# Optimization experiments

Measured on AMD Instinct MI355X. Metric: run time of the kernel, lower is better.

The kernel has to match this reference:

```python
import jax, jax.numpy as jnp
import numpy as np

N, G, S = 51200, 128, 400  # nodes, graphs, nodes-per-graph
E, IN, H, OUT = 819200, 128, 128, 10


def _graph_conv(x, src, dst, W_rel, b_rel, W_root):
    # PyG GraphConv (aggr='add'): lin_rel(sum_{j->i} x_j) + lin_root(x_i)
    agg = jax.ops.segment_sum(x[src], dst, num_segments=N)  # [N, d]
    return agg @ W_rel + b_rel + x @ W_root


def _mixup(x, lam, perm):
    return x * lam + (1.0 - lam) * x[perm]


def setup_inputs() -> dict:
    key = jax.random.key(0)
    ks = jax.random.split(key, 12)
    rng = np.random.default_rng(0)

    x0 = jax.random.normal(ks[0], (N, IN), dtype=jnp.float32)
    edge_index = jax.random.randint(ks[1], (2, E), 0, N, dtype=jnp.int64)
    lam = jax.random.uniform(ks[2], (1,), dtype=jnp.float32)
    ptr = jnp.arange(0, N + 1, S, dtype=jnp.int64)            # [G+1]
    batch = jnp.repeat(jnp.arange(G, dtype=jnp.int64), S)     # [N]

    def seg_perm():
        return jnp.asarray(np.concatenate(
            [g * S + rng.permutation(S) for g in range(G)]), dtype=jnp.int64)

    perm1, perm2, perm3 = seg_perm(), seg_perm(), seg_perm()

    def lin(k, fan_in, fan_out):
        bound = 1.0 / np.sqrt(fan_in)
        return jax.random.uniform(k, (fan_in, fan_out), jnp.float32, -bound, bound)

    params = {
        'W1_rel': lin(ks[3], IN, H), 'b1_rel': jnp.zeros((H,), jnp.float32),
        'W1_root': lin(ks[4], IN, H),
        'W2_rel': lin(ks[5], H, H), 'b2_rel': jnp.zeros((H,), jnp.float32),
        'W2_root': lin(ks[6], H, H),
        'W_lin': lin(ks[7], H, OUT), 'b_lin': jnp.zeros((OUT,), jnp.float32),
    }
    return dict(x0=x0, edge_index=edge_index, lam=lam, ptr=ptr, batch=batch,
                perm1=perm1, perm2=perm2, perm3=perm3, **params)


def reference(x0, edge_index, lam, ptr, batch, perm1, perm2, perm3,
              W1_rel, b1_rel, W1_root, W2_rel, b2_rel, W2_root, W_lin, b_lin):
    src, dst = edge_index[0], edge_index[1]
    l = lam[0]

    x1 = jax.nn.relu(_graph_conv(x0, src, dst, W1_rel, b1_rel, W1_root))
    x1 = _mixup(x1, l, perm1)  # dropout p=0.4 is identity in eval mode

    x2 = jax.nn.relu(_graph_conv(x1, src, dst, W2_rel, b2_rel, W2_root))
    x2 = _mixup(x2, l, perm2)

    # NOTE: original forward reuses conv2 for the third layer (conv3 unused)
    x3 = jax.nn.relu(_graph_conv(x2, src, dst, W2_rel, b2_rel, W2_root))
    x3 = _mixup(x3, l, perm3)

    pooled = jax.ops.segment_sum(x3, batch, num_segments=G)  # [G, H]
    logits = pooled @ W_lin + b_lin                          # [G, OUT]
    return jax.nn.log_softmax(logits, axis=-1)
```

## Files before the change

### kernel.cpp

```cpp
#include <hip/hip_runtime.h>

#define N_NODES 51200
#define N_EDGES 819200
#define HDIM 128
#define AK 256
#define NGRAPH 128
#define SEG 400
#define NOUT 10
#define SLOT 64

typedef unsigned short ushort_t;
typedef unsigned int uint_t;
typedef __attribute__((ext_vector_type(8))) short bf16x8;
typedef __attribute__((ext_vector_type(16))) float f32x16;

static __device__ __forceinline__ unsigned short f2bf(float f) {
    unsigned int u = __float_as_uint(f);
    unsigned int r = (u + 0x7fffu + ((u >> 16) & 1u)) >> 16;
    return (unsigned short)r;
}
static __device__ __forceinline__ float bf2f(unsigned short h) {
    return __uint_as_float(((unsigned int)h) << 16);
}


__global__ void k_scatter(const int* __restrict__ src, const int* __restrict__ dst,
                          int* __restrict__ cnt, ushort_t* __restrict__ col2) {
    int base = blockIdx.x * 1024 + threadIdx.x;
    int d[4], p[4];
#pragma unroll
    for (int k = 0; k < 4; ++k) d[k] = dst[base + k * 256];
#pragma unroll
    for (int k = 0; k < 4; ++k) p[k] = atomicAdd(&cnt[d[k]], 1);
#pragma unroll
    for (int k = 0; k < 4; ++k)
        col2[(size_t)d[k] * SLOT + p[k]] = (ushort_t)src[base + k * 256];
}


__global__ void k_prep(const float* __restrict__ x, ushort_t* __restrict__ Abuf,
                       const float* __restrict__ W1rel, const float* __restrict__ W1root,
                       const float* __restrict__ W2rel, const float* __restrict__ W2root,
                       ushort_t* __restrict__ Wfrag1, ushort_t* __restrict__ Wfrag2,
                       float* __restrict__ pooled) {
    int b = blockIdx.x;
    if (b < 6400) {
        int idx = b * 256 + threadIdx.x;
        int row = idx >> 5;
        int c4 = (idx & 31) * 4;
        float4 v = *(const float4*)(x + (size_t)row * HDIM + c4);
        ushort4 h;
        h.x = f2bf(v.x); h.y = f2bf(v.y); h.z = f2bf(v.z); h.w = f2bf(v.w);
        *(ushort4*)(Abuf + (size_t)row * AK + HDIM + c4) = h;
    } else if (b < 6656) {
        int w2 = (b >= 6528);
        int tid = (b - (w2 ? 6528 : 6400)) * 256 + threadIdx.x;
        const float* Wrel  = w2 ? W2rel : W1rel;
        const float* Wroot = w2 ? W2root : W1root;
        ushort_t* dstF     = w2 ? Wfrag2 : Wfrag1;
        int j = tid & 7;
        int l = (tid >> 3) & 63;
        int s = (tid >> 9) & 15;
        int t = tid >> 13;
        int k = 16 * s + (l >> 5) * 8 + j;
        int n = 32 * t + (l & 31);
        float v = (k < HDIM) ? Wrel[(size_t)k * HDIM + n]
                             : Wroot[(size_t)(k - HDIM) * HDIM + n];
        dstF[tid] = f2bf(v);
    } else {
        int i = (b - 6656) * 256 + threadIdx.x;
        pooled[i] = 0.f;
    }
}


__global__ __launch_bounds__(256) void k_aggregate(ushort_t* __restrict__ Abuf,
                                                   const int* __restrict__ cnt,
                                                   const ushort_t* __restrict__ col) {
    int wave = threadIdx.x >> 6;
    int lane = threadIdx.x & 63;
    int il = lane & 15;
    int qe = lane >> 4;
    int node = blockIdx.x * 4 + wave;
    int beg = node * SLOT;
    int end = beg + cnt[node];

    const ushort_t* xsrc = Abuf + HDIM + (size_t)il * 8;

    float a[4][8];
#pragma unroll
    for (int j = 0; j < 4; ++j)
#pragma unroll
        for (int k = 0; k < 8; ++k) a[j][k] = 0.f;

    int e = beg;
    for (; e + 16 <= end; e += 16) {
        int c[4];
#pragma unroll
        for (int j = 0; j < 4; ++j) c[j] = (int)col[e + 4 * j + qe];
#pragma unroll
        for (int j = 0; j < 4; ++j) {
            uint4 v = *(const uint4*)(xsrc + (size_t)c[j] * AK);
            a[j][0] += __uint_as_float(v.x << 16);
            a[j][1] += __uint_as_float(v.x & 0xffff0000u);
            a[j][2] += __uint_as_float(v.y << 16);
            a[j][3] += __uint_as_float(v.y & 0xffff0000u);
            a[j][4] += __uint_as_float(v.z << 16);
            a[j][5] += __uint_as_float(v.z & 0xffff0000u);
            a[j][6] += __uint_as_float(v.w << 16);
            a[j][7] += __uint_as_float(v.w & 0xffff0000u);
        }
    }
    for (; e + 4 <= end; e += 4) {
        int c = (int)col[e + qe];
        uint4 v = *(const uint4*)(xsrc + (size_t)c * AK);
        a[0][0] += __uint_as_float(v.x << 16);
        a[0][1] += __uint_as_float(v.x & 0xffff0000u);
        a[0][2] += __uint_as_float(v.y << 16);
        a[0][3] += __uint_as_float(v.y & 0xffff0000u);
        a[0][4] += __uint_as_float(v.z << 16);
        a[0][5] += __uint_as_float(v.z & 0xffff0000u);
        a[0][6] += __uint_as_float(v.w << 16);
        a[0][7] += __uint_as_float(v.w & 0xffff0000u);
    }
    if (e < end) {
        int idx = e + qe;
        bool ok = idx < end;
        int c = (int)col[ok ? idx : e];
        uint4 v = *(const uint4*)(xsrc + (size_t)c * AK);
        a[1][0] += ok ? __uint_as_float(v.x << 16) : 0.f;
        a[1][1] += ok ? __uint_as_float(v.x & 0xffff0000u) : 0.f;
        a[1][2] += ok ? __uint_as_float(v.y << 16) : 0.f;
        a[1][3] += ok ? __uint_as_float(v.y & 0xffff0000u) : 0.f;
        a[1][4] += ok ? __uint_as_float(v.z << 16) : 0.f;
        a[1][5] += ok ? __uint_as_float(v.z & 0xffff0000u) : 0.f;
        a[1][6] += ok ? __uint_as_float(v.w << 16) : 0.f;
        a[1][7] += ok ? __uint_as_float(v.w & 0xffff0000u) : 0.f;
    }

    float s[8];
#pragma unroll
    for (int k = 0; k < 8; ++k) {
        s[k] = (a[0][k] + a[1][k]) + (a[2][k] + a[3][k]);
        s[k] += __shfl_xor(s[k], 16);
        s[k] += __shfl_xor(s[k], 32);
    }

    if (qe == 0) {
        uint4 o;
        o.x = (uint_t)f2bf(s[0]) | ((uint_t)f2bf(s[1]) << 16);
        o.y = (uint_t)f2bf(s[2]) | ((uint_t)f2bf(s[3]) << 16);
        o.z = (uint_t)f2bf(s[4]) | ((uint_t)f2bf(s[5]) << 16);
        o.w = (uint_t)f2bf(s[6]) | ((uint_t)f2bf(s[7]) << 16);
        *(uint4*)(Abuf + (size_t)node * AK + il * 8) = o;
    }
}


__global__ __launch_bounds__(64) void k_gemm_mfma(const ushort_t* __restrict__ Abuf,
                                                  const ushort_t* __restrict__ Wfrag,
                                                  const float* __restrict__ bias,
                                                  ushort_t* __restrict__ y) {
    __shared__ ushort_t sm[32][72];
    int lane = threadIdx.x;
    int nh = blockIdx.x & 1;
    int row0 = (blockIdx.x >> 1) * 32;
    int m = lane & 31;
    int half = lane >> 5;

    f32x16 acc[2];
#pragma unroll
    for (int t = 0; t < 2; ++t) acc[t] = (f32x16)(0.f);

    float bb[2];
#pragma unroll
    for (int t = 0; t < 2; ++t) bb[t] = bias[nh * 64 + t * 32 + m];

    const ushort_t* arow = Abuf + (size_t)(row0 + m) * AK + half * 8;
    const ushort_t* wf = Wfrag + (size_t)lane * 8 + (size_t)nh * 2 * 16 * 512;

#pragma unroll
    for (int s = 0; s < 16; ++s) {
        bf16x8 afrag = *(const bf16x8*)(arow + s * 16);
#pragma unroll
        for (int t = 0; t < 2; ++t) {
            bf16x8 bfrag = *(const bf16x8*)(wf + (size_t)(t * 16 + s) * 512);
            acc[t] = __builtin_amdgcn_mfma_f32_32x32x16_bf16(afrag, bfrag, acc[t], 0, 0, 0);
        }
    }

#pragma unroll
    for (int t = 0; t < 2; ++t) {
#pragma unroll
        for (int r = 0; r < 16; ++r) {
            int rowL = (r & 3) + 8 * (r >> 2) + 4 * half;
            sm[rowL][t * 32 + m] = f2bf(fmaxf(acc[t][r] + bb[t], 0.f));
        }
    }
    __syncthreads();
    int seg = lane & 7;
    int rbase = lane >> 3;
#pragma unroll
    for (int it = 0; it < 4; ++it) {
        int rowL = rbase + it * 8;
        int4 chunk = *(const int4*)&sm[rowL][seg * 8];
        *(int4*)(y + (size_t)(row0 + rowL) * HDIM + nh * 64 + seg * 8) = chunk;
    }
}


__global__ __launch_bounds__(64) void k_gemm_pool(const ushort_t* __restrict__ Abuf,
                                                  const ushort_t* __restrict__ Wfrag,
                                                  const float* __restrict__ bias,
                                                  float* __restrict__ pooled) {
    int lane = threadIdx.x;
    int nh = blockIdx.x & 1;
    int row0 = (blockIdx.x >> 1) * 32;
    int m = lane & 31;
    int half = lane >> 5;

    f32x16 acc[2];
#pragma unroll
    for (int t = 0; t < 2; ++t) acc[t] = (f32x16)(0.f);

    float bb[2];
#pragma unroll
    for (int t = 0; t < 2; ++t) bb[t] = bias[nh * 64 + t * 32 + m];

    const ushort_t* arow = Abuf + (size_t)(row0 + m) * AK + half * 8;
    const ushort_t* wf = Wfrag + (size_t)lane * 8 + (size_t)nh * 2 * 16 * 512;

#pragma unroll
    for (int s = 0; s < 16; ++s) {
        bf16x8 afrag = *(const bf16x8*)(arow + s * 16);
#pragma unroll
        for (int t = 0; t < 2; ++t) {
            bf16x8 bfrag = *(const bf16x8*)(wf + (size_t)(t * 16 + s) * 512);
            acc[t] = __builtin_amdgcn_mfma_f32_32x32x16_bf16(afrag, bfrag, acc[t], 0, 0, 0);
        }
    }

    int g0 = row0 / SEG;
    int bnd = (g0 + 1) * SEG;
    int straddle = (row0 + 31 >= bnd);

#pragma unroll
    for (int t = 0; t < 2; ++t) {
        float s0 = 0.f, s1 = 0.f;
#pragma unroll
        for (int r = 0; r < 16; ++r) {
            int row = row0 + (r & 3) + 8 * (r >> 2) + 4 * half;
            float v = fmaxf(acc[t][r] + bb[t], 0.f);
            if (row < bnd) s0 += v; else s1 += v;
        }
        s0 += __shfl_xor(s0, 32);
        s1 += __shfl_xor(s1, 32);
        if (half == 0) {
            int coln = nh * 64 + t * 32 + m;
            atomicAdd(&pooled[g0 * HDIM + coln], s0);
            if (straddle) atomicAdd(&pooled[(g0 + 1) * HDIM + coln], s1);
        }
    }
}


__global__ void k_mixup_toA(const ushort_t* __restrict__ y, const int* __restrict__ perm,
                            const float* __restrict__ lam, ushort_t* __restrict__ Abuf) {
    int idx = blockIdx.x * 256 + threadIdx.x;
    int row = idx >> 5;
    int c4 = (idx & 31) * 4;
    float l = lam[0];
    float om = 1.f - l;
    int p = perm[row];
    ushort4 a = *(const ushort4*)(y + (size_t)row * HDIM + c4);
    ushort4 b = *(const ushort4*)(y + (size_t)p * HDIM + c4);
    ushort4 o;
    o.x = f2bf(l * bf2f(a.x) + om * bf2f(b.x));
    o.y = f2bf(l * bf2f(a.y) + om * bf2f(b.y));
    o.z = f2bf(l * bf2f(a.z) + om * bf2f(b.z));
    o.w = f2bf(l * bf2f(a.w) + om * bf2f(b.w));
    *(ushort4*)(Abuf + (size_t)row * AK + HDIM + c4) = o;
}


__global__ __launch_bounds__(64) void k_final(const float* __restrict__ pooled,
                                              const float* __restrict__ Wlin,
                                              const float* __restrict__ blin,
                                              float* __restrict__ out) {
    int g = blockIdx.x;
    int lane = threadIdx.x;
    float2 v = *(const float2*)(pooled + (size_t)g * HDIM + lane * 2);
    float p[NOUT];
#pragma unroll
    for (int o = 0; o < NOUT; ++o)
        p[o] = v.x * Wlin[(size_t)(2 * lane) * NOUT + o] +
               v.y * Wlin[(size_t)(2 * lane + 1) * NOUT + o];
#pragma unroll
    for (int mask = 1; mask < 64; mask <<= 1)
#pragma unroll
        for (int o = 0; o < NOUT; ++o) p[o] += __shfl_xor(p[o], mask);
    if (lane == 0) {
        float lg[NOUT];
        float mx = -1e30f;
#pragma unroll
        for (int o = 0; o < NOUT; ++o) { lg[o] = p[o] + blin[o]; mx = fmaxf(mx, lg[o]); }
        float se = 0.f;
#pragma unroll
        for (int o = 0; o < NOUT; ++o) se += expf(lg[o] - mx);
        float lse = mx + logf(se);
#pragma unroll
        for (int o = 0; o < NOUT; ++o) out[g * NOUT + o] = lg[o] - lse;
    }
}


extern "C" void kernel_launch(void* const* d_in, const int* in_sizes, int n_in,
                              void* d_out, int out_size, void* d_ws, size_t ws_size,
                              hipStream_t stream) {
    const float* x0     = (const float*)d_in[0];
    const int*   edge   = (const int*)d_in[1];
    const int*   src    = edge;
    const int*   dst    = edge + N_EDGES;
    const float* lam    = (const float*)d_in[2];
    const int*   perm1  = (const int*)d_in[5];
    const int*   perm2  = (const int*)d_in[6];
    const float* W1_rel = (const float*)d_in[8];
    const float* b1_rel = (const float*)d_in[9];
    const float* W1_root= (const float*)d_in[10];
    const float* W2_rel = (const float*)d_in[11];
    const float* b2_rel = (const float*)d_in[12];
    const float* W2_root= (const float*)d_in[13];
    const float* W_lin  = (const float*)d_in[14];
    const float* b_lin  = (const float*)d_in[15];
    float* out = (float*)d_out;

    char* w = (char*)d_ws;
    size_t off = 0;
    auto alloc = [&](size_t bytes) -> void* {
        void* p = w + off;
        off = (off + bytes + 255) & ~(size_t)255;
        return p;
    };
    int* cnt       = (int*)alloc((size_t)N_NODES * 4);
    ushort_t* col2 = (ushort_t*)alloc((size_t)N_NODES * SLOT * 2);
    ushort_t* Abuf   = (ushort_t*)alloc((size_t)N_NODES * AK * 2);
    ushort_t* ybuf   = (ushort_t*)alloc((size_t)N_NODES * HDIM * 2);
    ushort_t* Wfrag1 = (ushort_t*)alloc(32768 * 2);
    ushort_t* Wfrag2 = (ushort_t*)alloc(32768 * 2);
    float* pooled    = (float*)alloc((size_t)NGRAPH * HDIM * 4);

    hipMemsetAsync(cnt, 0, (size_t)N_NODES * 4, stream);

    k_scatter<<<N_EDGES / 1024, 256, 0, stream>>>(src, dst, cnt, col2);

    k_prep<<<6720, 256, 0, stream>>>(x0, Abuf, W1_rel, W1_root, W2_rel, W2_root,
                                     Wfrag1, Wfrag2, pooled);

    const int aggGrid  = N_NODES / 4;
    const int gemmGrid = (N_NODES / 32) * 2;
    const int elGrid   = (N_NODES * HDIM / 4) / 256;

    k_aggregate<<<aggGrid, 256, 0, stream>>>(Abuf, cnt, col2);
    k_gemm_mfma<<<gemmGrid, 64, 0, stream>>>(Abuf, Wfrag1, b1_rel, ybuf);
    k_mixup_toA<<<elGrid, 256, 0, stream>>>(ybuf, perm1, lam, Abuf);
    k_aggregate<<<aggGrid, 256, 0, stream>>>(Abuf, cnt, col2);
    k_gemm_mfma<<<gemmGrid, 64, 0, stream>>>(Abuf, Wfrag2, b2_rel, ybuf);
    k_mixup_toA<<<elGrid, 256, 0, stream>>>(ybuf, perm2, lam, Abuf);
    k_aggregate<<<aggGrid, 256, 0, stream>>>(Abuf, cnt, col2);
    k_gemm_pool<<<gemmGrid, 64, 0, stream>>>(Abuf, Wfrag2, b2_rel, pooled);

    k_final<<<NGRAPH, 64, 0, stream>>>(pooled, W_lin, b_lin, out);
}
```

Measured before the change: 302.2 us.

## Fuse neighbor aggregation into GEMM kernel via shared memory tile

Merges the per-layer aggregation and MFMA GEMM into one kernel: each 256-thread block aggregates 32 nodes into an LDS tile, then two waves run the GEMM reading the aggregated half from LDS and the root half from a compact 128-wide activation buffer. This removes the round trip of aggregated features through global memory, shrinks the gathered feature rows from a 256-wide to a 128-wide buffer, and cuts kernel launches. The cnt memset is folded into the prep kernel. The trade-off is that half the waves sit idle during the GEMM phase and each block now serialises 8 nodes per wave for the gather.

```diff
diff --git a/kernel.cpp b/kernel.cpp
--- a/kernel.cpp
+++ b/kernel.cpp
@@ -3,11 +3,11 @@
 #define N_NODES 51200
 #define N_EDGES 819200
 #define HDIM 128
-#define AK 256
 #define NGRAPH 128
 #define SEG 400
 #define NOUT 10
 #define SLOT 64
+#define PAD 136
 
 typedef unsigned short ushort_t;
 typedef unsigned int uint_t;
@@ -38,11 +38,11 @@
 }
 
 
-__global__ void k_prep(const float* __restrict__ x, ushort_t* __restrict__ Abuf,
+__global__ void k_prep(const float* __restrict__ x, ushort_t* __restrict__ xin,
                        const float* __restrict__ W1rel, const float* __restrict__ W1root,
                        const float* __restrict__ W2rel, const float* __restrict__ W2root,
                        ushort_t* __restrict__ Wfrag1, ushort_t* __restrict__ Wfrag2,
-                       float* __restrict__ pooled) {
+                       float* __restrict__ pooled, int* __restrict__ cnt) {
     int b = blockIdx.x;
     if (b < 6400) {
         int idx = b * 256 + threadIdx.x;
@@ -51,7 +51,7 @@
         float4 v = *(const float4*)(x + (size_t)row * HDIM + c4);
         ushort4 h;
         h.x = f2bf(v.x); h.y = f2bf(v.y); h.z = f2bf(v.z); h.w = f2bf(v.w);
-        *(ushort4*)(Abuf + (size_t)row * AK + HDIM + c4) = h;
+        *(ushort4*)(xin + (size_t)row * HDIM + c4) = h;
     } else if (b < 6656) {
         int w2 = (b >= 6528);
         int tid = (b - (w2 ? 6528 : 6400)) * 256 + threadIdx.x;
@@ -67,205 +67,314 @@
         float v = (k < HDIM) ? Wrel[(size_t)k * HDIM + n]
                              : Wroot[(size_t)(k - HDIM) * HDIM + n];
         dstF[tid] = f2bf(v);
-    } else {
+    } else if (b < 6720) {
         int i = (b - 6656) * 256 + threadIdx.x;
         pooled[i] = 0.f;
-    }
-}
-
-
-__global__ __launch_bounds__(256) void k_aggregate(ushort_t* __restrict__ Abuf,
-                                                   const int* __restrict__ cnt,
-                                                   const ushort_t* __restrict__ col) {
-    int wave = threadIdx.x >> 6;
+    } else {
+        int i = (b - 6720) * 256 + threadIdx.x;
+        cnt[i] = 0;
+    }
+}
+
+
+__global__ __launch_bounds__(256) void k_layer(const ushort_t* __restrict__ xin,
+                                               const int* __restrict__ cnt,
+                                               const ushort_t* __restrict__ col,
+                                               const ushort_t* __restrict__ Wfrag,
+                                               const float* __restrict__ bias,
+                                               ushort_t* __restrict__ y) {
+    __shared__ ushort_t sm[32][PAD];
+    __shared__ ushort_t smy[2][32][72];
+    int wv = threadIdx.x >> 6;
     int lane = threadIdx.x & 63;
-    int il = lane & 15;
-    int qe = lane >> 4;
-    int node = blockIdx.x * 4 + wave;
-    int beg = node * SLOT;
-    int end = beg + cnt[node];
-
-    const ushort_t* xsrc = Abuf + HDIM + (size_t)il * 8;
-
-    float a[4][8];
-#pragma unroll
-    for (int j = 0; j < 4; ++j)
-#pragma unroll
-        for (int k = 0; k < 8; ++k) a[j][k] = 0.f;
-
-    int e = beg;
-    for (; e + 16 <= end; e += 16) {
-        int c[4];
-#pragma unroll
-        for (int j = 0; j < 4; ++j) c[j] = (int)col[e + 4 * j + qe];
-#pragma unroll
-        for (int j = 0; j < 4; ++j) {
-            uint4 v = *(const uint4*)(xsrc + (size_t)c[j] * AK);
-            a[j][0] += __uint_as_float(v.x << 16);
-            a[j][1] += __uint_as_float(v.x & 0xffff0000u);
-            a[j][2] += __uint_as_float(v.y << 16);
-            a[j][3] += __uint_as_float(v.y & 0xffff0000u);
-            a[j][4] += __uint_as_float(v.z << 16);
-            a[j][5] += __uint_as_float(v.z & 0xffff0000u);
-            a[j][6] += __uint_as_float(v.w << 16);
-            a[j][7] += __uint_as_float(v.w & 0xffff0000u);
-        }
-    }
-    for (; e + 4 <= end; e += 4) {
-        int c = (int)col[e + qe];
-        uint4 v = *(const uint4*)(xsrc + (size_t)c * AK);
-        a[0][0] += __uint_as_float(v.x << 16);
-        a[0][1] += __uint_as_float(v.x & 0xffff0000u);
-        a[0][2] += __uint_as_float(v.y << 16);
-        a[0][3] += __uint_as_float(v.y & 0xffff0000u);
-        a[0][4] += __uint_as_float(v.z << 16);
-        a[0][5] += __uint_as_float(v.z & 0xffff0000u);
-        a[0][6] += __uint_as_float(v.w << 16);
-        a[0][7] += __uint_as_float(v.w & 0xffff0000u);
-    }
-    if (e < end) {
-        int idx = e + qe;
-        bool ok = idx < end;
-        int c = (int)col[ok ? idx : e];
-        uint4 v = *(const uint4*)(xsrc + (size_t)c * AK);
-        a[1][0] += ok ? __uint_as_float(v.x << 16) : 0.f;
-        a[1][1] += ok ? __uint_as_float(v.x & 0xffff0000u) : 0.f;
-        a[1][2] += ok ? __uint_as_float(v.y << 16) : 0.f;
-        a[1][3] += ok ? __uint_as_float(v.y & 0xffff0000u) : 0.f;
-        a[1][4] += ok ? __uint_as_float(v.z << 16) : 0.f;
-        a[1][5] += ok ? __uint_as_float(v.z & 0xffff0000u) : 0.f;
-        a[1][6] += ok ? __uint_as_float(v.w << 16) : 0.f;
-        a[1][7] += ok ? __uint_as_float(v.w & 0xffff0000u) : 0.f;
-    }
-
-    float s[8];
-#pragma unroll
-    for (int k = 0; k < 8; ++k) {
-        s[k] = (a[0][k] + a[1][k]) + (a[2][k] + a[3][k]);
-        s[k] += __shfl_xor(s[k], 16);
-        s[k] += __shfl_xor(s[k], 32);
-    }
-
-    if (qe == 0) {
-        uint4 o;
-        o.x = (uint_t)f2bf(s[0]) | ((uint_t)f2bf(s[1]) << 16);
-        o.y = (uint_t)f2bf(s[2]) | ((uint_t)f2bf(s[3]) << 16);
-        o.z = (uint_t)f2bf(s[4]) | ((uint_t)f2bf(s[5]) << 16);
-        o.w = (uint_t)f2bf(s[6]) | ((uint_t)f2bf(s[7]) << 16);
-        *(uint4*)(Abuf + (size_t)node * AK + il * 8) = o;
-    }
-}
-
-
-__global__ __launch_bounds__(64) void k_gemm_mfma(const ushort_t* __restrict__ Abuf,
-                                                  const ushort_t* __restrict__ Wfrag,
-                                                  const float* __restrict__ bias,
-                                                  ushort_t* __restrict__ y) {
-    __shared__ ushort_t sm[32][72];
-    int lane = threadIdx.x;
-    int nh = blockIdx.x & 1;
-    int row0 = (blockIdx.x >> 1) * 32;
-    int m = lane & 31;
-    int half = lane >> 5;
-
-    f32x16 acc[2];
-#pragma unroll
-    for (int t = 0; t < 2; ++t) acc[t] = (f32x16)(0.f);
-
-    float bb[2];
-#pragma unroll
-    for (int t = 0; t < 2; ++t) bb[t] = bias[nh * 64 + t * 32 + m];
-
-    const ushort_t* arow = Abuf + (size_t)(row0 + m) * AK + half * 8;
-    const ushort_t* wf = Wfrag + (size_t)lane * 8 + (size_t)nh * 2 * 16 * 512;
-
-#pragma unroll
-    for (int s = 0; s < 16; ++s) {
-        bf16x8 afrag = *(const bf16x8*)(arow + s * 16);
+    int row0 = blockIdx.x * 32;
+
+    {
+        int il = lane & 15;
+        int qe = lane >> 4;
+        const ushort_t* xsrc = xin + (size_t)il * 8;
+        for (int i = 0; i < 8; ++i) {
+            int r = wv + i * 4;
+            int node = row0 + r;
+            int beg = node * SLOT;
+            int end = beg + cnt[node];
+
+            float a[4][8];
+#pragma unroll
+            for (int j = 0; j < 4; ++j)
+#pragma unroll
+                for (int k = 0; k < 8; ++k) a[j][k] = 0.f;
+
+            int e = beg;
+            for (; e + 16 <= end; e += 16) {
+                int c[4];
+#pragma unroll
+                for (int j = 0; j < 4; ++j) c[j] = (int)col[e + 4 * j + qe];
+#pragma unroll
+                for (int j = 0; j < 4; ++j) {
+                    uint4 v = *(const uint4*)(xsrc + (size_t)c[j] * HDIM);
+                    a[j][0] += __uint_as_float(v.x << 16);
+                    a[j][1] += __uint_as_float(v.x & 0xffff0000u);
+                    a[j][2] += __uint_as_float(v.y << 16);
+                    a[j][3] += __uint_as_float(v.y & 0xffff0000u);
+                    a[j][4] += __uint_as_float(v.z << 16);
+                    a[j][5] += __uint_as_float(v.z & 0xffff0000u);
+                    a[j][6] += __uint_as_float(v.w << 16);
+                    a[j][7] += __uint_as_float(v.w & 0xffff0000u);
+                }
+            }
+            for (; e + 4 <= end; e += 4) {
+                int c = (int)col[e + qe];
+                uint4 v = *(const uint4*)(xsrc + (size_t)c * HDIM);
+                a[0][0] += __uint_as_float(v.x << 16);
+                a[0][1] += __uint_as_float(v.x & 0xffff0000u);
+                a[0][2] += __uint_as_float(v.y << 16);
+                a[0][3] += __uint_as_float(v.y & 0xffff0000u);
+                a[0][4] += __uint_as_float(v.z << 16);
+                a[0][5] += __uint_as_float(v.z & 0xffff0000u);
+                a[0][6] += __uint_as_float(v.w << 16);
+                a[0][7] += __uint_as_float(v.w & 0xffff0000u);
+            }
+            if (e < end) {
+                int idx = e + qe;
+                bool ok = idx < end;
+                int c = (int)col[ok ? idx : e];
+                uint4 v = *(const uint4*)(xsrc + (size_t)c * HDIM);
+                a[1][0] += ok ? __uint_as_float(v.x << 16) : 0.f;
+                a[1][1] += ok ? __uint_as_float(v.x & 0xffff0000u) : 0.f;
+                a[1][2] += ok ? __uint_as_float(v.y << 16) : 0.f;
+                a[1][3] += ok ? __uint_as_float(v.y & 0xffff0000u) : 0.f;
+                a[1][4] += ok ? __uint_as_float(v.z << 16) : 0.f;
+                a[1][5] += ok ? __uint_as_float(v.z & 0xffff0000u) : 0.f;
+                a[1][6] += ok ? __uint_as_float(v.w << 16) : 0.f;
+                a[1][7] += ok ? __uint_as_float(v.w & 0xffff0000u) : 0.f;
+            }
+
+            float s[8];
+#pragma unroll
+            for (int k = 0; k < 8; ++k) {
+                s[k] = (a[0][k] + a[1][k]) + (a[2][k] + a[3][k]);
+                s[k] += __shfl_xor(s[k], 16);
+                s[k] += __shfl_xor(s[k], 32);
+            }
+            if (qe == 0) {
+                uint4 o;
+                o.x = (uint_t)f2bf(s[0]) | ((uint_t)f2bf(s[1]) << 16);
+                o.y = (uint_t)f2bf(s[2]) | ((uint_t)f2bf(s[3]) << 16);
+                o.z = (uint_t)f2bf(s[4]) | ((uint_t)f2bf(s[5]) << 16);
+                o.w = (uint_t)f2bf(s[6]) | ((uint_t)f2bf(s[7]) << 16);
+                *(uint4*)&sm[r][il * 8] = o;
+            }
+        }
+    }
+    __syncthreads();
+
+    if (wv < 2) {
+        int nh = wv;
+        int m = lane & 31;
+        int half = lane >> 5;
+
+        f32x16 acc[2];
+#pragma unroll
+        for (int t = 0; t < 2; ++t) acc[t] = (f32x16)(0.f);
+        float bb[2];
+#pragma unroll
+        for (int t = 0; t < 2; ++t) bb[t] = bias[nh * 64 + t * 32 + m];
+
+        const ushort_t* wf = Wfrag + (size_t)lane * 8 + (size_t)nh * 2 * 16 * 512;
+        const ushort_t* arow = xin + (size_t)(row0 + m) * HDIM + half * 8;
+
+#pragma unroll
+        for (int s = 0; s < 8; ++s) {
+            bf16x8 afrag = *(const bf16x8*)&sm[m][s * 16 + half * 8];
+#pragma unroll
+            for (int t = 0; t < 2; ++t) {
+                bf16x8 bfrag = *(const bf16x8*)(wf + (size_t)(t * 16 + s) * 512);
+                acc[t] = __builtin_amdgcn_mfma_f32_32x32x16_bf16(afrag, bfrag, acc[t], 0, 0, 0);
+            }
+        }
+#pragma unroll
+        for (int s = 8; s < 16; ++s) {
+            bf16x8 afrag = *(const bf16x8*)(arow + (s - 8) * 16);
+#pragma unroll
+            for (int t = 0; t < 2; ++t) {
+                bf16x8 bfrag = *(const bf16x8*)(wf + (size_t)(t * 16 + s) * 512);
+                acc[t] = __builtin_amdgcn_mfma_f32_32x32x16_bf16(afrag, bfrag, acc[t], 0, 0, 0);
+            }
+        }
+
 #pragma unroll
         for (int t = 0; t < 2; ++t) {
-            bf16x8 bfrag = *(const bf16x8*)(wf + (size_t)(t * 16 + s) * 512);
-            acc[t] = __builtin_amdgcn_mfma_f32_32x32x16_bf16(afrag, bfrag, acc[t], 0, 0, 0);
-        }
-    }
-
-#pragma unroll
-    for (int t = 0; t < 2; ++t) {
-#pragma unroll
-        for (int r = 0; r < 16; ++r) {
-            int rowL = (r & 3) + 8 * (r >> 2) + 4 * half;
-            sm[rowL][t * 32 + m] = f2bf(fmaxf(acc[t][r] + bb[t], 0.f));
+#pragma unroll
+            for (int r = 0; r < 16; ++r) {
+                int rowL = (r & 3) + 8 * (r >> 2) + 4 * half;
+                smy[nh][rowL][t * 32 + m] = f2bf(fmaxf(acc[t][r] + bb[t], 0.f));
+            }
+        }
+        int seg = lane & 7;
+        int rbase = lane >> 3;
+#pragma unroll
+        for (int it = 0; it < 4; ++it) {
+            int rowL = rbase + it * 8;
+            int4 chunk = *(const int4*)&smy[nh][rowL][seg * 8];
+            *(int4*)(y + (size_t)(row0 + rowL) * HDIM + nh * 64 + seg * 8) = chunk;
+        }
+    }
+}
+
+
+__global__ __launch_bounds__(256) void k_layer_pool(const ushort_t* __restrict__ xin,
+                                                    const int* __restrict__ cnt,
+                                                    const ushort_t* __restrict__ col,
+                                                    const ushort_t* __restrict__ Wfrag,
+                                                    const float* __restrict__ bias,
+                                                    float* __restrict__ pooled) {
+    __shared__ ushort_t sm[32][PAD];
+    int wv = threadIdx.x >> 6;
+    int lane = threadIdx.x & 63;
+    int row0 = blockIdx.x * 32;
+
+    {
+        int il = lane & 15;
+        int qe = lane >> 4;
+        const ushort_t* xsrc = xin + (size_t)il * 8;
+        for (int i = 0; i < 8; ++i) {
+            int r = wv + i * 4;
+            int node = row0 + r;
+            int beg = node * SLOT;
+            int end = beg + cnt[node];
+
+            float a[4][8];
+#pragma unroll
+            for (int j = 0; j < 4; ++j)
+#pragma unroll
+                for (int k = 0; k < 8; ++k) a[j][k] = 0.f;
+
+            int e = beg;
+            for (; e + 16 <= end; e += 16) {
+                int c[4];
+#pragma unroll
+                for (int j = 0; j < 4; ++j) c[j] = (int)col[e + 4 * j + qe];
+#pragma unroll
+                for (int j = 0; j < 4; ++j) {
+                    uint4 v = *(const uint4*)(xsrc + (size_t)c[j] * HDIM);
+                    a[j][0] += __uint_as_float(v.x << 16);
+                    a[j][1] += __uint_as_float(v.x & 0xffff0000u);
+                    a[j][2] += __uint_as_float(v.y << 16);
+                    a[j][3] += __uint_as_float(v.y & 0xffff0000u);
+                    a[j][4] += __uint_as_float(v.z << 16);
+                    a[j][5] += __uint_as_float(v.z & 0xffff0000u);
+                    a[j][6] += __uint_as_float(v.w << 16);
+                    a[j][7] += __uint_as_float(v.w & 0xffff0000u);
+                }
+            }
+            for (; e + 4 <= end; e += 4) {
+                int c = (int)col[e + qe];
+                uint4 v = *(const uint4*)(xsrc + (size_t)c * HDIM);
+                a[0][0] += __uint_as_float(v.x << 16);
+                a[0][1] += __uint_as_float(v.x & 0xffff0000u);
+                a[0][2] += __uint_as_float(v.y << 16);
+                a[0][3] += __uint_as_float(v.y & 0xffff0000u);
+                a[0][4] += __uint_as_float(v.z << 16);
+                a[0][5] += __uint_as_float(v.z & 0xffff0000u);
+                a[0][6] += __uint_as_float(v.w << 16);
+                a[0][7] += __uint_as_float(v.w & 0xffff0000u);
+            }
+            if (e < end) {
+                int idx = e + qe;
+                bool ok = idx < end;
+                int c = (int)col[ok ? idx : e];
+                uint4 v = *(const uint4*)(xsrc + (size_t)c * HDIM);
+                a[1][0] += ok ? __uint_as_float(v.x << 16) : 0.f;
+                a[1][1] += ok ? __uint_as_float(v.x & 0xffff0000u) : 0.f;
+                a[1][2] += ok ? __uint_as_float(v.y << 16) : 0.f;
+                a[1][3] += ok ? __uint_as_float(v.y & 0xffff0000u) : 0.f;
+                a[1][4] += ok ? __uint_as_float(v.z << 16) : 0.f;
+                a[1][5] += ok ? __uint_as_float(v.z & 0xffff0000u) : 0.f;
+                a[1][6] += ok ? __uint_as_float(v.w << 16) : 0.f;
+                a[1][7] += ok ? __uint_as_float(v.w & 0xffff0000u) : 0.f;
+            }
+
+            float s[8];
+#pragma unroll
+            for (int k = 0; k < 8; ++k) {
+                s[k] = (a[0][k] + a[1][k]) + (a[2][k] + a[3][k]);
+                s[k] += __shfl_xor(s[k], 16);
+                s[k] += __shfl_xor(s[k], 32);
+            }
+            if (qe == 0) {
+                uint4 o;
+                o.x = (uint_t)f2bf(s[0]) | ((uint_t)f2bf(s[1]) << 16);
+                o.y = (uint_t)f2bf(s[2]) | ((uint_t)f2bf(s[3]) << 16);
+                o.z = (uint_t)f2bf(s[4]) | ((uint_t)f2bf(s[5]) << 16);
+                o.w = (uint_t)f2bf(s[6]) | ((uint_t)f2bf(s[7]) << 16);
+                *(uint4*)&sm[r][il * 8] = o;
+            }
         }
     }
     __syncthreads();
-    int seg = lane & 7;
-    int rbase = lane >> 3;
-#pragma unroll
-    for (int it = 0; it < 4; ++it) {
-        int rowL = rbase + it * 8;
-        int4 chunk = *(const int4*)&sm[rowL][seg * 8];
-        *(int4*)(y + (size_t)(row0 + rowL) * HDIM + nh * 64 + seg * 8) = chunk;
-    }
-}
-
-
-__global__ __launch_bounds__(64) void k_gemm_pool(const ushort_t* __restrict__ Abuf,
-                                                  const ushort_t* __restrict__ Wfrag,
-                                                  const float* __restrict__ bias,
-                                                  float* __restrict__ pooled) {
-    int lane = threadIdx.x;
-    int nh = blockIdx.x & 1;
-    int row0 = (blockIdx.x >> 1) * 32;
-    int m = lane & 31;
-    int half = lane >> 5;
-
-    f32x16 acc[2];
-#pragma unroll
-    for (int t = 0; t < 2; ++t) acc[t] = (f32x16)(0.f);
-
-    float bb[2];
-#pragma unroll
-    for (int t = 0; t < 2; ++t) bb[t] = bias[nh * 64 + t * 32 + m];
-
-    const ushort_t* arow = Abuf + (size_t)(row0 + m) * AK + half * 8;
-    const ushort_t* wf = Wfrag + (size_t)lane * 8 + (size_t)nh * 2 * 16 * 512;
-
-#pragma unroll
-    for (int s = 0; s < 16; ++s) {
-        bf16x8 afrag = *(const bf16x8*)(arow + s * 16);
+
+    if (wv < 2) {
+        int nh = wv;
+        int m = lane & 31;
+        int half = lane >> 5;
+
+        f32x16 acc[2];
+#pragma unroll
+        for (int t = 0; t < 2; ++t) acc[t] = (f32x16)(0.f);
+        float bb[2];
+#pragma unroll
+        for (int t = 0; t < 2; ++t) bb[t] = bias[nh * 64 + t * 32 + m];
+
+        const ushort_t* wf = Wfrag + (size_t)lane * 8 + (size_t)nh * 2 * 16 * 512;
+        const ushort_t* arow = xin + (size_t)(row0 + m) * HDIM + half * 8;
+
+#pragma unroll
+        for (int s = 0; s < 8; ++s) {
+            bf16x8 afrag = *(const bf16x8*)&sm[m][s * 16 + half * 8];
+#pragma unroll
+            for (int t = 0; t < 2; ++t) {
+                bf16x8 bfrag = *(const bf16x8*)(wf + (size_t)(t * 16 + s) * 512);
+                acc[t] = __builtin_amdgcn_mfma_f32_32x32x16_bf16(afrag, bfrag, acc[t], 0, 0, 0);
+            }
+        }
+#pragma unroll
+        for (int s = 8; s < 16; ++s) {
+            bf16x8 afrag = *(const bf16x8*)(arow + (s - 8) * 16);
+#pragma unroll
+            for (int t = 0; t < 2; ++t) {
+                bf16x8 bfrag = *(const bf16x8*)(wf + (size_t)(t * 16 + s) * 512);
+                acc[t] = __builtin_amdgcn_mfma_f32_32x32x16_bf16(afrag, bfrag, acc[t], 0, 0, 0);
+            }
+        }
+
+        int g0 = row0 / SEG;
+        int bnd = (g0 + 1) * SEG;
+        int straddle = (row0 + 31 >= bnd);
+
 #pragma unroll
         for (int t = 0; t < 2; ++t) {
-            bf16x8 bfrag = *(const bf16x8*)(wf + (size_t)(t * 16 + s) * 512);
-            acc[t] = __builtin_amdgcn_mfma_f32_32x32x16_bf16(afrag, bfrag, acc[t], 0, 0, 0);
-        }
-    }
-
-    int g0 = row0 / SEG;
-    int bnd = (g0 + 1) * SEG;
-    int straddle = (row0 + 31 >= bnd);
-
-#pragma unroll
-    for (int t = 0; t < 2; ++t) {
-        float s0 = 0.f, s1 = 0.f;
-#pragma unroll
-        for (int r = 0; r < 16; ++r) {
-            int row = row0 + (r & 3) + 8 * (r >> 2) + 4 * half;
-            float v = fmaxf(acc[t][r] + bb[t], 0.f);
-            if (row < bnd) s0 += v; else s1 += v;
-        }
-        s0 += __shfl_xor(s0, 32);
-        s1 += __shfl_xor(s1, 32);
-        if (half == 0) {
-            int coln = nh * 64 + t * 32 + m;
-            atomicAdd(&pooled[g0 * HDIM + coln], s0);
-            if (straddle) atomicAdd(&pooled[(g0 + 1) * HDIM + coln], s1);
-        }
-    }
-}
-
-
-__global__ void k_mixup_toA(const ushort_t* __restrict__ y, const int* __restrict__ perm,
-                            const float* __restrict__ lam, ushort_t* __restrict__ Abuf) {
+            float s0 = 0.f, s1 = 0.f;
+#pragma unroll
+            for (int r = 0; r < 16; ++r) {
+                int row = row0 + (r & 3) + 8 * (r >> 2) + 4 * half;
+                float v = fmaxf(acc[t][r] + bb[t], 0.f);
+                if (row < bnd) s0 += v; else s1 += v;
+            }
+            s0 += __shfl_xor(s0, 32);
+            s1 += __shfl_xor(s1, 32);
+            if (half == 0) {
+                int coln = nh * 64 + t * 32 + m;
+                atomicAdd(&pooled[g0 * HDIM + coln], s0);
+                if (straddle) atomicAdd(&pooled[(g0 + 1) * HDIM + coln], s1);
+            }
+        }
+    }
+}
+
+
+__global__ void k_mixup(const ushort_t* __restrict__ y, const int* __restrict__ perm,
+                        const float* __restrict__ lam, ushort_t* __restrict__ xin) {
     int idx = blockIdx.x * 256 + threadIdx.x;
     int row = idx >> 5;
     int c4 = (idx & 31) * 4;
@@ -279,7 +388,7 @@
     o.y = f2bf(l * bf2f(a.y) + om * bf2f(b.y));
     o.z = f2bf(l * bf2f(a.z) + om * bf2f(b.z));
     o.w = f2bf(l * bf2f(a.w) + om * bf2f(b.w));
-    *(ushort4*)(Abuf + (size_t)row * AK + HDIM + c4) = o;
+    *(ushort4*)(xin + (size_t)row * HDIM + c4) = o;
 }
 
 
@@ -343,31 +452,24 @@
     };
     int* cnt       = (int*)alloc((size_t)N_NODES * 4);
     ushort_t* col2 = (ushort_t*)alloc((size_t)N_NODES * SLOT * 2);
-    ushort_t* Abuf   = (ushort_t*)alloc((size_t)N_NODES * AK * 2);
+    ushort_t* xin    = (ushort_t*)alloc((size_t)N_NODES * HDIM * 2);
     ushort_t* ybuf   = (ushort_t*)alloc((size_t)N_NODES * HDIM * 2);
     ushort_t* Wfrag1 = (ushort_t*)alloc(32768 * 2);
     ushort_t* Wfrag2 = (ushort_t*)alloc(32768 * 2);
     float* pooled    = (float*)alloc((size_t)NGRAPH * HDIM * 4);
 
-    hipMemsetAsync(cnt, 0, (size_t)N_NODES * 4, stream);
-
+    k_prep<<<6920, 256, 0, stream>>>(x0, xin, W1_rel, W1_root, W2_rel, W2_root,
+                                     Wfrag1, Wfrag2, pooled, cnt);
     k_scatter<<<N_EDGES / 1024, 256, 0, stream>>>(src, dst, cnt, col2);
 
-    k_prep<<<6720, 256, 0, stream>>>(x0, Abuf, W1_rel, W1_root, W2_rel, W2_root,
-                                     Wfrag1, Wfrag2, pooled);
-
-    const int aggGrid  = N_NODES / 4;
-    const int gemmGrid = (N_NODES / 32) * 2;
-    const int elGrid   = (N_NODES * HDIM / 4) / 256;
-
-    k_aggregate<<<aggGrid, 256, 0, stream>>>(Abuf, cnt, col2);
-    k_gemm_mfma<<<gemmGrid, 64, 0, stream>>>(Abuf, Wfrag1, b1_rel, ybuf);
-    k_mixup_toA<<<elGrid, 256, 0, stream>>>(ybuf, perm1, lam, Abuf);
-    k_aggregate<<<aggGrid, 256, 0, stream>>>(Abuf, cnt, col2);
-    k_gemm_mfma<<<gemmGrid, 64, 0, stream>>>(Abuf, Wfrag2, b2_rel, ybuf);
-    k_mixup_toA<<<elGrid, 256, 0, stream>>>(ybuf, perm2, lam, Abuf);
-    k_aggregate<<<aggGrid, 256, 0, stream>>>(Abuf, cnt, col2);
-    k_gemm_pool<<<gemmGrid, 64, 0, stream>>>(Abuf, Wfrag2, b2_rel, pooled);
+    const int layerGrid = N_NODES / 32;
+    const int elGrid    = (N_NODES * HDIM / 4) / 256;
+
+    k_layer<<<layerGrid, 256, 0, stream>>>(xin, cnt, col2, Wfrag1, b1_rel, ybuf);
+    k_mixup<<<elGrid, 256, 0, stream>>>(ybuf, perm1, lam, xin);
+    k_layer<<<layerGrid, 256, 0, stream>>>(xin, cnt, col2, Wfrag2, b2_rel, ybuf);
+    k_mixup<<<elGrid, 256, 0, stream>>>(ybuf, perm2, lam, xin);
+    k_layer_pool<<<layerGrid, 256, 0, stream>>>(xin, cnt, col2, Wfrag2, b2_rel, pooled);
 
     k_final<<<NGRAPH, 64, 0, stream>>>(pooled, W_lin, b_lin, out);
 }
```

Result: slower. 335.3 us (+11.0%).
